# Kernel tuning notes

Measured on AMD Instinct MI355X. Metric: run time of the kernel, lower is better.

Reference implementation:

```python
import jax, jax.numpy as jnp
import numpy as np

QDIM = 32
H = 512
B = 65536
BIAS = 2.0
N_TRIL = QDIM * (QDIM + 1) // 2  # 528 total params per sample
TRIL_R, TRIL_C = np.tril_indices(QDIM, -1)  # strictly-lower entries (500)
DIAG = np.arange(QDIM)


def setup_inputs() -> dict:
    key = jax.random.key(0)
    ks = jax.random.split(key, 12)
    def lin(k, fan_in, fan_out):
        return jax.random.normal(k, (fan_in, fan_out), dtype=jnp.float32) / np.sqrt(fan_in).astype(np.float32)
    return {
        "q": jax.random.normal(ks[0], (B, QDIM), dtype=jnp.float32),
        # ResMLP embed: input linear, two residual hidden blocks, output linear
        "W_in": lin(ks[1], QDIM, H), "b_in": jnp.zeros((H,), jnp.float32),
        "W_h1": lin(ks[2], H, H),    "b_h1": jnp.zeros((H,), jnp.float32),
        "W_h2": lin(ks[3], H, H),    "b_h2": jnp.zeros((H,), jnp.float32),
        "W_out": lin(ks[4], H, H),   "b_out": jnp.zeros((H,), jnp.float32),
        # Cholesky parameter head: H -> qdim*(qdim+1)/2
        "W_o": lin(ks[5], H, N_TRIL), "b_o": jnp.zeros((N_TRIL,), jnp.float32),
    }


def reference(q, W_in, b_in, W_h1, b_h1, W_h2, b_h2, W_out, b_out, W_o, b_o):
    # ResMLP embed (relu, residual connections on equal-width hidden layers)
    x = jax.nn.relu(q @ W_in + b_in)               # [B, H]
    x = jax.nn.relu(x @ W_h1 + b_h1) + x           # residual block 1
    x = jax.nn.relu(x @ W_h2 + b_h2) + x           # residual block 2
    embed = x @ W_out + b_out                      # [B, H]
    # Cholesky factor params
    L_params = embed @ W_o + b_o                   # [B, 528]
    L_diag = L_params[:, :QDIM] + BIAS             # [B, 32]
    L_tril = L_params[:, QDIM:]                    # [B, 496+... strictly lower]
    Bsz = q.shape[0]
    L = jnp.zeros((Bsz, QDIM, QDIM), L_params.dtype)
    L = L.at[:, TRIL_R, TRIL_C].set(L_tril)        # bfill_lowertriangle
    L = L.at[:, DIAG, DIAG].set(L_diag)            # bfill_diagonal
    M = L @ jnp.swapaxes(L, -1, -2)                # SPD mass matrix [B, 32, 32]
    return M
```

## Files before the change

### kernel.cpp

```cpp
#include <hip/hip_runtime.h>
#include <math.h>

typedef __bf16 bf16;
typedef bf16 bf16x2 __attribute__((ext_vector_type(2)));
typedef bf16 bf16x4 __attribute__((ext_vector_type(4)));
typedef bf16 bf16x8 __attribute__((ext_vector_type(8)));
typedef float f32x4 __attribute__((ext_vector_type(4)));

#define BATCH 65536
#define QD 32
#define HD 512
#define NT 528
#define BM 64
#define BIAS_C 2.0f

#define OFF_WIN  0
#define OFF_WH1  16384
#define OFF_WH2  278528
#define OFF_WOUT 540672
#define OFF_WO   802816
#define WT_TOTAL 1073152
#define N_TILES  2096

#define MFMA(a, b, c) __builtin_amdgcn_mfma_f32_16x16x32_bf16((a), (b), (c), 0, 0, 0)

__global__ __launch_bounds__(256) void prep_weights(
    const float* __restrict__ W_in, const float* __restrict__ W_h1,
    const float* __restrict__ W_h2, const float* __restrict__ W_out,
    const float* __restrict__ W_o, bf16* __restrict__ wt)
{
    const int bt = blockIdx.x;

    __shared__ float lds[32][17];
    const float* src; int ld, nt, kt;
    if (bt < 32)        { src = W_in;                 nt = bt;     kt = 0;      ld = HD; }
    else if (bt < 544)  { int t = bt - 32;   src = W_h1;  nt = t >> 4; kt = t & 15; ld = HD; }
    else if (bt < 1056) { int t = bt - 544;  src = W_h2;  nt = t >> 4; kt = t & 15; ld = HD; }
    else if (bt < 1568) { int t = bt - 1056; src = W_out; nt = t >> 4; kt = t & 15; ld = HD; }
    else                { int t = bt - 1568; src = W_o;   nt = t >> 4; kt = t & 15; ld = NT; }

    const int s = threadIdx.x * 2;
    {
        int ki = s >> 4, fi = s & 15;
        const float* p = src + (size_t)(kt * 32 + ki) * ld + nt * 16 + fi;
        lds[ki][fi]     = p[0];
        lds[ki][fi + 1] = p[1];
    }
    __syncthreads();
    {
        int fi = s >> 5, ki = s & 31;
        bf16x2 w;
        w[0] = (bf16)lds[ki][fi];
        w[1] = (bf16)lds[ki + 1][fi];
        *(bf16x2*)(wt + (size_t)bt * 512 + s) = w;
    }
}

__device__ __forceinline__ int xbyte(int m, int f) {
    return m * 1024 + ((((f >> 3)) ^ m) << 4) + ((f & 7) << 1);
}

__device__ __forceinline__ int lbyte(int il, int r, int c) {
    int ch = (c >> 3) ^ (r & 3) ^ ((r >> 2) & 3) ^ (il & 3);
    int by = (c & 7) ^ ((il >> 2) << 1);
    return il * 2048 + r * 64 + (ch << 4) + (by << 1);
}

__device__ __forceinline__ void p2rc(int p, int& r_, int& c_) {
    int t = p - QD;
    int r = 0;
    #pragma unroll
    for (int b = 16; b; b >>= 1) {
        int cand = r + b;
        int tri = (int)(((unsigned)(cand * (cand - 1))) >> 1);
        if (tri <= t) r = cand;
    }
    int c = t - (int)(((unsigned)(r * (r - 1))) >> 1);
    if (p < QD) { r_ = p; c_ = p; }
    else        { r_ = r; c_ = c; }
}

__global__ __launch_bounds__(512) __attribute__((amdgpu_waves_per_eu(4, 4)))
void fused_kernel(
    const float* __restrict__ q,
    const float* __restrict__ b_in, const float* __restrict__ b_h1,
    const float* __restrict__ b_h2, const float* __restrict__ b_out,
    const float* __restrict__ b_o,
    const bf16* __restrict__ wt, float* __restrict__ out)
{
    __shared__ __attribute__((aligned(16))) unsigned char smem[65536];
    const int tid  = threadIdx.x;
    const int lane = tid & 63;
    const int wave = tid >> 6;
    const int l15  = lane & 15;
    const int quad = lane >> 4;
    const int blk  = blockIdx.x;

    const f32x4 zf = {0.f, 0.f, 0.f, 0.f};
    f32x4 acc[4][4];

    {
        bf16x8 bfr[4];
        #pragma unroll
        for (int ct = 0; ct < 4; ++ct) {
            const float* qp = q + (size_t)(blk * 64 + ct * 16 + l15) * QD + quad * 8;
            f32x4 lo = *(const f32x4*)qp;
            f32x4 hi = *(const f32x4*)(qp + 4);
            bf16x8 b;
            #pragma unroll
            for (int j = 0; j < 4; ++j) { b[j] = (bf16)lo[j]; b[4 + j] = (bf16)hi[j]; }
            bfr[ct] = b;
        }
        #pragma unroll
        for (int rt = 0; rt < 4; ++rt) {
            bf16x8 a = *(const bf16x8*)(wt + OFF_WIN + (wave * 4 + rt) * 512 + l15 * 32 + quad * 8);
            #pragma unroll
            for (int ct = 0; ct < 4; ++ct)
                acc[rt][ct] = MFMA(a, bfr[ct], zf);
        }
        #pragma unroll
        for (int rt = 0; rt < 4; ++rt) {
            int f0 = wave * 64 + rt * 16 + quad * 4;
            f32x4 bias = *(const f32x4*)(b_in + f0);
            #pragma unroll
            for (int ct = 0; ct < 4; ++ct) {
                int m = ct * 16 + l15;
                bf16x4 w;
                #pragma unroll
                for (int r = 0; r < 4; ++r) {
                    float v = acc[rt][ct][r] + bias[r];
                    v = v > 0.f ? v : 0.f;
                    w[r] = (bf16)v;
                }
                *(bf16x4*)(smem + xbyte(m, f0)) = w;
            }
        }
    }
    __syncthreads();

    const bf16*  WL[3] = { wt + OFF_WH1, wt + OFF_WH2, wt + OFF_WOUT };
    const float* BL[3] = { b_h1, b_h2, b_out };
    #pragma unroll
    for (int L = 0; L < 3; ++L) {
        #pragma unroll
        for (int rt = 0; rt < 4; ++rt)
            #pragma unroll
            for (int ct = 0; ct < 4; ++ct)
                acc[rt][ct] = zf;
        const bf16* W = WL[L];
        #pragma unroll 2
        for (int kk = 0; kk < 16; ++kk) {
            bf16x8 bfr2[4];
            #pragma unroll
            for (int ct = 0; ct < 4; ++ct) {
                int m = ct * 16 + l15;
                bfr2[ct] = *(const bf16x8*)(smem + m * 1024 + (((kk * 4 + quad) ^ m) << 4));
            }
            #pragma unroll
            for (int rt = 0; rt < 4; ++rt) {
                bf16x8 a = *(const bf16x8*)(W + ((wave * 4 + rt) * 16 + kk) * 512 + l15 * 32 + quad * 8);
                #pragma unroll
                for (int ct = 0; ct < 4; ++ct)
                    acc[rt][ct] = MFMA(a, bfr2[ct], acc[rt][ct]);
            }
        }
        __syncthreads();
        {
            const float* Bv = BL[L];
            #pragma unroll
            for (int rt = 0; rt < 4; ++rt) {
                int f0 = wave * 64 + rt * 16 + quad * 4;
                f32x4 bias = *(const f32x4*)(Bv + f0);
                #pragma unroll
                for (int ct = 0; ct < 4; ++ct) {
                    int m = ct * 16 + l15;
                    unsigned char* p = smem + xbyte(m, f0);
                    bf16x4 w;
                    if (L < 2) {
                        bf16x4 old = *(const bf16x4*)p;
                        #pragma unroll
                        for (int r = 0; r < 4; ++r) {
                            float v = acc[rt][ct][r] + bias[r];
                            v = v > 0.f ? v : 0.f;
                            v += (float)old[r];
                            w[r] = (bf16)v;
                        }
                    } else {
                        #pragma unroll
                        for (int r = 0; r < 4; ++r) {
                            float v = acc[rt][ct][r] + bias[r];
                            w[r] = (bf16)v;
                        }
                    }
                    *(bf16x4*)p = w;
                }
            }
        }
        __syncthreads();
    }

    f32x4 acc_ex = zf;
    #pragma unroll
    for (int rt = 0; rt < 4; ++rt)
        #pragma unroll
        for (int ct = 0; ct < 4; ++ct)
            acc[rt][ct] = zf;
    #pragma unroll 2
    for (int kk = 0; kk < 16; ++kk) {
        bf16x8 bfr2[4];
        #pragma unroll
        for (int ct = 0; ct < 4; ++ct) {
            int m = ct * 16 + l15;
            bfr2[ct] = *(const bf16x8*)(smem + m * 1024 + (((kk * 4 + quad) ^ m) << 4));
        }
        #pragma unroll
        for (int rt = 0; rt < 4; ++rt) {
            bf16x8 a = *(const bf16x8*)(wt + OFF_WO + ((wave * 4 + rt) * 16 + kk) * 512 + l15 * 32 + quad * 8);
            #pragma unroll
            for (int ct = 0; ct < 4; ++ct)
                acc[rt][ct] = MFMA(a, bfr2[ct], acc[rt][ct]);
        }
        if (wave >= 4) {
            bf16x8 aex = *(const bf16x8*)(wt + OFF_WO + (32 * 16 + kk) * 512 + l15 * 32 + quad * 8);
            if (wave == 4) acc_ex = MFMA(aex, bfr2[0], acc_ex);
            else if (wave == 5) acc_ex = MFMA(aex, bfr2[1], acc_ex);
            else if (wave == 6) acc_ex = MFMA(aex, bfr2[2], acc_ex);
            else acc_ex = MFMA(aex, bfr2[3], acc_ex);
        }
    }
    __syncthreads();

    #pragma unroll
    for (int rt = 0; rt < 4; ++rt) {
        f32x4 b = *(const f32x4*)(b_o + wave * 64 + rt * 16 + quad * 4);
        if (rt < 2 && wave == 0) {
            #pragma unroll
            for (int r = 0; r < 4; ++r) b[r] += BIAS_C;
        }
        #pragma unroll
        for (int ct = 0; ct < 4; ++ct)
            #pragma unroll
            for (int r = 0; r < 4; ++r)
                acc[rt][ct][r] += b[r];
    }
    if (wave >= 4) {
        f32x4 be = *(const f32x4*)(b_o + 512 + quad * 4);
        #pragma unroll
        for (int r = 0; r < 4; ++r) acc_ex[r] += be[r];
    }

    int loff[4][4];
    #pragma unroll
    for (int rt = 0; rt < 4; ++rt)
        #pragma unroll
        for (int r = 0; r < 4; ++r) {
            int rr, cc;
            p2rc(wave * 64 + rt * 16 + quad * 4 + r, rr, cc);
            loff[rt][r] = lbyte(l15, rr, cc);
        }
    int loffex[4] = {0, 0, 0, 0};
    if (wave >= 4) {
        #pragma unroll
        for (int r = 0; r < 4; ++r) {
            int rr, cc;
            p2rc(512 + quad * 4 + r, rr, cc);
            loffex[r] = lbyte(l15, rr, cc);
        }
    }

    {
        unsigned long long* z = (unsigned long long*)smem;
        #pragma unroll
        for (int i = 0; i < 16; ++i) z[tid + 512 * i] = 0ull;
    }
    __syncthreads();

    #pragma unroll
    for (int g = 0; g < 4; ++g) {
        #pragma unroll
        for (int rt = 0; rt < 4; ++rt) {
            #pragma unroll
            for (int r = 0; r < 4; ++r) {
                float v = acc[rt][g][r];
                bf16 hi = (bf16)v;
                bf16 lo = (bf16)(v - (float)hi);
                int off = loff[rt][r];
                *(bf16*)(smem + off) = hi;
                *(bf16*)(smem + 32768 + off) = lo;
            }
        }
        if (wave == 4 + g) {
            #pragma unroll
            for (int r = 0; r < 4; ++r) {
                float v = acc_ex[r];
                bf16 hi = (bf16)v;
                bf16 lo = (bf16)(v - (float)hi);
                int off = loffex[r];
                *(bf16*)(smem + off) = hi;
                *(bf16*)(smem + 32768 + off) = lo;
            }
        }
        __syncthreads();
        #pragma unroll
        for (int ii = 0; ii < 2; ++ii) {
            const int it = wave + ii * 8;
            bf16x8 Fh[2], Fl[2];
            #pragma unroll
            for (int tl = 0; tl < 2; ++tl) {
                int m = tl * 16 + l15;
                int ch = quad ^ (m & 3) ^ ((m >> 2) & 3) ^ (it & 3);
                int off = it * 2048 + m * 64 + (ch << 4);
                Fh[tl] = *(const bf16x8*)(smem + off);
                Fl[tl] = *(const bf16x8*)(smem + 32768 + off);
            }
            long base = ((long)(blk * 64 + g * 16 + it)) * 1024;
            #pragma unroll
            for (int mt = 0; mt < 2; ++mt) {
                #pragma unroll
                for (int nt = 0; nt < 2; ++nt) {
                    f32x4 mm = MFMA(Fh[mt], Fh[nt], zf);
                    mm = MFMA(Fh[mt], Fl[nt], mm);
                    mm = MFMA(Fl[mt], Fh[nt], mm);
                    #pragma unroll
                    for (int r = 0; r < 4; ++r)
                        out[base + (long)(mt * 16 + quad * 4 + r) * 32 + nt * 16 + l15] = mm[r];
                }
            }
        }
        __syncthreads();
    }
}

extern "C" void kernel_launch(void* const* d_in, const int* in_sizes, int n_in,
                              void* d_out, int out_size, void* d_ws, size_t ws_size,
                              hipStream_t stream)
{
    const float* q     = (const float*)d_in[0];
    const float* W_in  = (const float*)d_in[1];
    const float* b_in  = (const float*)d_in[2];
    const float* W_h1  = (const float*)d_in[3];
    const float* b_h1  = (const float*)d_in[4];
    const float* W_h2  = (const float*)d_in[5];
    const float* b_h2  = (const float*)d_in[6];
    const float* W_out = (const float*)d_in[7];
    const float* b_out = (const float*)d_in[8];
    const float* W_o   = (const float*)d_in[9];
    const float* b_o   = (const float*)d_in[10];
    float* out = (float*)d_out;
    bf16* wt = (bf16*)d_ws;

    prep_weights<<<N_TILES, 256, 0, stream>>>(W_in, W_h1, W_h2, W_out, W_o, wt);
    fused_kernel<<<BATCH / BM, 512, 0, stream>>>(q, b_in, b_h1, b_h2, b_out, b_o, wt, out);
}
```

Measured before the change: 453.5 us.

## Double batch tile to 128 rows with 16 waves per block

Each block now handles 128 samples using 1024 threads and 128KB of LDS, with each wave computing 32 output features across 8 column tiles instead of 64 features across 4. The goal is to halve how often each weight tile is reloaded from global memory/L2 per sample, since weights are read once per block. The cost is a larger LDS footprint and block size, which limits blocks per CU, plus more LDS reads of activations per MFMA. The Cholesky stage and the extra-column handling are remapped to 16 waves.

```diff
diff --git a/kernel.cpp b/kernel.cpp
--- a/kernel.cpp
+++ b/kernel.cpp
@@ -11,7 +11,7 @@
 #define QD 32
 #define HD 512
 #define NT 528
-#define BM 64
+#define BM 128
 #define BIAS_C 2.0f
 
 #define OFF_WIN  0
@@ -57,7 +57,7 @@
 }
 
 __device__ __forceinline__ int xbyte(int m, int f) {
-    return m * 1024 + ((((f >> 3)) ^ m) << 4) + ((f & 7) << 1);
+    return m * 1024 + ((((f >> 3)) ^ (m & 63)) << 4) + ((f & 7) << 1);
 }
 
 __device__ __forceinline__ int lbyte(int il, int r, int c) {
@@ -80,7 +80,7 @@
     else        { r_ = r; c_ = c; }
 }
 
-__global__ __launch_bounds__(512) __attribute__((amdgpu_waves_per_eu(4, 4)))
+__global__ __launch_bounds__(1024) __attribute__((amdgpu_waves_per_eu(4, 4)))
 void fused_kernel(
     const float* __restrict__ q,
     const float* __restrict__ b_in, const float* __restrict__ b_h1,
@@ -88,7 +88,7 @@
     const float* __restrict__ b_o,
     const bf16* __restrict__ wt, float* __restrict__ out)
 {
-    __shared__ __attribute__((aligned(16))) unsigned char smem[65536];
+    __shared__ __attribute__((aligned(16))) unsigned char smem[131072];
     const int tid  = threadIdx.x;
     const int lane = tid & 63;
     const int wave = tid >> 6;
@@ -97,33 +97,31 @@
     const int blk  = blockIdx.x;
 
     const f32x4 zf = {0.f, 0.f, 0.f, 0.f};
-    f32x4 acc[4][4];
+    f32x4 acc[2][8];
 
     {
-        bf16x8 bfr[4];
-        #pragma unroll
-        for (int ct = 0; ct < 4; ++ct) {
-            const float* qp = q + (size_t)(blk * 64 + ct * 16 + l15) * QD + quad * 8;
+        bf16x8 aA[2];
+        #pragma unroll
+        for (int rt = 0; rt < 2; ++rt)
+            aA[rt] = *(const bf16x8*)(wt + OFF_WIN + (wave * 2 + rt) * 512 + l15 * 32 + quad * 8);
+        #pragma unroll
+        for (int ct = 0; ct < 8; ++ct) {
+            const float* qp = q + (size_t)(blk * BM + ct * 16 + l15) * QD + quad * 8;
             f32x4 lo = *(const f32x4*)qp;
             f32x4 hi = *(const f32x4*)(qp + 4);
             bf16x8 b;
             #pragma unroll
             for (int j = 0; j < 4; ++j) { b[j] = (bf16)lo[j]; b[4 + j] = (bf16)hi[j]; }
-            bfr[ct] = b;
-        }
-        #pragma unroll
-        for (int rt = 0; rt < 4; ++rt) {
-            bf16x8 a = *(const bf16x8*)(wt + OFF_WIN + (wave * 4 + rt) * 512 + l15 * 32 + quad * 8);
-            #pragma unroll
-            for (int ct = 0; ct < 4; ++ct)
-                acc[rt][ct] = MFMA(a, bfr[ct], zf);
-        }
-        #pragma unroll
-        for (int rt = 0; rt < 4; ++rt) {
-            int f0 = wave * 64 + rt * 16 + quad * 4;
+            #pragma unroll
+            for (int rt = 0; rt < 2; ++rt)
+                acc[rt][ct] = MFMA(aA[rt], b, zf);
+        }
+        #pragma unroll
+        for (int rt = 0; rt < 2; ++rt) {
+            int f0 = wave * 32 + rt * 16 + quad * 4;
             f32x4 bias = *(const f32x4*)(b_in + f0);
             #pragma unroll
-            for (int ct = 0; ct < 4; ++ct) {
+            for (int ct = 0; ct < 8; ++ct) {
                 int m = ct * 16 + l15;
                 bf16x4 w;
                 #pragma unroll
@@ -143,36 +141,32 @@
     #pragma unroll
     for (int L = 0; L < 3; ++L) {
         #pragma unroll
-        for (int rt = 0; rt < 4; ++rt)
-            #pragma unroll
-            for (int ct = 0; ct < 4; ++ct)
+        for (int rt = 0; rt < 2; ++rt)
+            #pragma unroll
+            for (int ct = 0; ct < 8; ++ct)
                 acc[rt][ct] = zf;
         const bf16* W = WL[L];
         #pragma unroll 2
         for (int kk = 0; kk < 16; ++kk) {
-            bf16x8 bfr2[4];
-            #pragma unroll
-            for (int ct = 0; ct < 4; ++ct) {
+            bf16x8 a0 = *(const bf16x8*)(W + ((wave * 2 + 0) * 16 + kk) * 512 + l15 * 32 + quad * 8);
+            bf16x8 a1 = *(const bf16x8*)(W + ((wave * 2 + 1) * 16 + kk) * 512 + l15 * 32 + quad * 8);
+            #pragma unroll
+            for (int ct = 0; ct < 8; ++ct) {
                 int m = ct * 16 + l15;
-                bfr2[ct] = *(const bf16x8*)(smem + m * 1024 + (((kk * 4 + quad) ^ m) << 4));
-            }
-            #pragma unroll
-            for (int rt = 0; rt < 4; ++rt) {
-                bf16x8 a = *(const bf16x8*)(W + ((wave * 4 + rt) * 16 + kk) * 512 + l15 * 32 + quad * 8);
-                #pragma unroll
-                for (int ct = 0; ct < 4; ++ct)
-                    acc[rt][ct] = MFMA(a, bfr2[ct], acc[rt][ct]);
+                bf16x8 b = *(const bf16x8*)(smem + m * 1024 + (((kk * 4 + quad) ^ (m & 63)) << 4));
+                acc[0][ct] = MFMA(a0, b, acc[0][ct]);
+                acc[1][ct] = MFMA(a1, b, acc[1][ct]);
             }
         }
         __syncthreads();
         {
             const float* Bv = BL[L];
             #pragma unroll
-            for (int rt = 0; rt < 4; ++rt) {
-                int f0 = wave * 64 + rt * 16 + quad * 4;
+            for (int rt = 0; rt < 2; ++rt) {
+                int f0 = wave * 32 + rt * 16 + quad * 4;
                 f32x4 bias = *(const f32x4*)(Bv + f0);
                 #pragma unroll
-                for (int ct = 0; ct < 4; ++ct) {
+                for (int ct = 0; ct < 8; ++ct) {
                     int m = ct * 16 + l15;
                     unsigned char* p = smem + xbyte(m, f0);
                     bf16x4 w;
@@ -201,65 +195,60 @@
 
     f32x4 acc_ex = zf;
     #pragma unroll
-    for (int rt = 0; rt < 4; ++rt)
-        #pragma unroll
-        for (int ct = 0; ct < 4; ++ct)
+    for (int rt = 0; rt < 2; ++rt)
+        #pragma unroll
+        for (int ct = 0; ct < 8; ++ct)
             acc[rt][ct] = zf;
     #pragma unroll 2
     for (int kk = 0; kk < 16; ++kk) {
-        bf16x8 bfr2[4];
-        #pragma unroll
-        for (int ct = 0; ct < 4; ++ct) {
+        bf16x8 a0 = *(const bf16x8*)(wt + OFF_WO + ((wave * 2 + 0) * 16 + kk) * 512 + l15 * 32 + quad * 8);
+        bf16x8 a1 = *(const bf16x8*)(wt + OFF_WO + ((wave * 2 + 1) * 16 + kk) * 512 + l15 * 32 + quad * 8);
+        #pragma unroll
+        for (int ct = 0; ct < 8; ++ct) {
             int m = ct * 16 + l15;
-            bfr2[ct] = *(const bf16x8*)(smem + m * 1024 + (((kk * 4 + quad) ^ m) << 4));
-        }
-        #pragma unroll
-        for (int rt = 0; rt < 4; ++rt) {
-            bf16x8 a = *(const bf16x8*)(wt + OFF_WO + ((wave * 4 + rt) * 16 + kk) * 512 + l15 * 32 + quad * 8);
-            #pragma unroll
-            for (int ct = 0; ct < 4; ++ct)
-                acc[rt][ct] = MFMA(a, bfr2[ct], acc[rt][ct]);
-        }
-        if (wave >= 4) {
+            bf16x8 b = *(const bf16x8*)(smem + m * 1024 + (((kk * 4 + quad) ^ (m & 63)) << 4));
+            acc[0][ct] = MFMA(a0, b, acc[0][ct]);
+            acc[1][ct] = MFMA(a1, b, acc[1][ct]);
+        }
+        if (wave >= 8) {
             bf16x8 aex = *(const bf16x8*)(wt + OFF_WO + (32 * 16 + kk) * 512 + l15 * 32 + quad * 8);
-            if (wave == 4) acc_ex = MFMA(aex, bfr2[0], acc_ex);
-            else if (wave == 5) acc_ex = MFMA(aex, bfr2[1], acc_ex);
-            else if (wave == 6) acc_ex = MFMA(aex, bfr2[2], acc_ex);
-            else acc_ex = MFMA(aex, bfr2[3], acc_ex);
+            int mex = (wave - 8) * 16 + l15;
+            bf16x8 bex = *(const bf16x8*)(smem + mex * 1024 + (((kk * 4 + quad) ^ (mex & 63)) << 4));
+            acc_ex = MFMA(aex, bex, acc_ex);
         }
     }
     __syncthreads();
 
     #pragma unroll
-    for (int rt = 0; rt < 4; ++rt) {
-        f32x4 b = *(const f32x4*)(b_o + wave * 64 + rt * 16 + quad * 4);
-        if (rt < 2 && wave == 0) {
+    for (int rt = 0; rt < 2; ++rt) {
+        f32x4 b = *(const f32x4*)(b_o + wave * 32 + rt * 16 + quad * 4);
+        if (wave == 0) {
             #pragma unroll
             for (int r = 0; r < 4; ++r) b[r] += BIAS_C;
         }
         #pragma unroll
-        for (int ct = 0; ct < 4; ++ct)
+        for (int ct = 0; ct < 8; ++ct)
             #pragma unroll
             for (int r = 0; r < 4; ++r)
                 acc[rt][ct][r] += b[r];
     }
-    if (wave >= 4) {
+    if (wave >= 8) {
         f32x4 be = *(const f32x4*)(b_o + 512 + quad * 4);
         #pragma unroll
         for (int r = 0; r < 4; ++r) acc_ex[r] += be[r];
     }
 
-    int loff[4][4];
-    #pragma unroll
-    for (int rt = 0; rt < 4; ++rt)
+    int loff[2][4];
+    #pragma unroll
+    for (int rt = 0; rt < 2; ++rt)
         #pragma unroll
         for (int r = 0; r < 4; ++r) {
             int rr, cc;
-            p2rc(wave * 64 + rt * 16 + quad * 4 + r, rr, cc);
+            p2rc(wave * 32 + rt * 16 + quad * 4 + r, rr, cc);
             loff[rt][r] = lbyte(l15, rr, cc);
         }
     int loffex[4] = {0, 0, 0, 0};
-    if (wave >= 4) {
+    if (wave >= 8) {
         #pragma unroll
         for (int r = 0; r < 4; ++r) {
             int rr, cc;
@@ -271,14 +260,14 @@
     {
         unsigned long long* z = (unsigned long long*)smem;
         #pragma unroll
-        for (int i = 0; i < 16; ++i) z[tid + 512 * i] = 0ull;
+        for (int i = 0; i < 8; ++i) z[tid + 1024 * i] = 0ull;
     }
     __syncthreads();
 
     #pragma unroll
-    for (int g = 0; g < 4; ++g) {
-        #pragma unroll
-        for (int rt = 0; rt < 4; ++rt) {
+    for (int g = 0; g < 8; ++g) {
+        #pragma unroll
+        for (int rt = 0; rt < 2; ++rt) {
             #pragma unroll
             for (int r = 0; r < 4; ++r) {
                 float v = acc[rt][g][r];
@@ -289,7 +278,7 @@
                 *(bf16*)(smem + 32768 + off) = lo;
             }
         }
-        if (wave == 4 + g) {
+        if (wave == 8 + g) {
             #pragma unroll
             for (int r = 0; r < 4; ++r) {
                 float v = acc_ex[r];
@@ -301,9 +290,8 @@
             }
         }
         __syncthreads();
-        #pragma unroll
-        for (int ii = 0; ii < 2; ++ii) {
-            const int it = wave + ii * 8;
+        {
+            const int it = wave;
             bf16x8 Fh[2], Fl[2];
             #pragma unroll
             for (int tl = 0; tl < 2; ++tl) {
@@ -313,7 +301,7 @@
                 Fh[tl] = *(const bf16x8*)(smem + off);
                 Fl[tl] = *(const bf16x8*)(smem + 32768 + off);
             }
-            long base = ((long)(blk * 64 + g * 16 + it)) * 1024;
+            long base = ((long)(blk * BM + g * 16 + it)) * 1024;
             #pragma unroll
             for (int mt = 0; mt < 2; ++mt) {
                 #pragma unroll
@@ -350,5 +338,5 @@
     bf16* wt = (bf16*)d_ws;
 
     prep_weights<<<N_TILES, 256, 0, stream>>>(W_in, W_h1, W_h2, W_out, W_o, wt);
-    fused_kernel<<<BATCH / BM, 512, 0, stream>>>(q, b_in, b_h1, b_h2, b_out, b_o, wt, out);
-}
+    fused_kernel<<<BATCH / BM, 1024, 0, stream>>>(q, b_in, b_h1, b_h2, b_out, b_o, wt, out);
+}
```

Result: faster. 421.0 us (-7.2%).
